# Kernel optimization log

Measured on AMD Instinct MI355X. Metric: run time of the kernel, lower is better.

Reference implementation:

```python
import jax, jax.numpy as jnp
import numpy as np

V = 50000
K = 24
NB = 10
P = (K - 1) * 9  # 207 pose-blend coefficients
# canonical SMPL kinematic tree (parent[0] is unused / root)
SMPL_PARENT = np.array([0, 0, 0, 0, 1, 2, 3, 4, 5, 6, 7, 8, 9, 9, 9, 12, 13, 14, 16, 17, 18, 19, 20, 21], dtype=np.int64)


def setup_inputs() -> dict:
    key = jax.random.key(0)
    ks = jax.random.split(key, 8)
    betas = jax.random.normal(ks[0], (NB,), dtype=jnp.float32)
    pose = jax.random.normal(ks[1], (K, 3), dtype=jnp.float32) * 0.3
    trans = jax.random.normal(ks[2], (3,), dtype=jnp.float32)
    shapedirs = jax.random.normal(ks[3], (V, 3, NB), dtype=jnp.float32) * 0.01
    v_template = jax.random.normal(ks[4], (V, 3), dtype=jnp.float32)
    J_regressor = jax.random.uniform(ks[5], (K, V), dtype=jnp.float32)
    J_regressor = J_regressor / jnp.sum(J_regressor, axis=1, keepdims=True)
    weights = jax.random.uniform(ks[6], (V, K), dtype=jnp.float32)
    weights = weights / jnp.sum(weights, axis=1, keepdims=True)
    posedirs = jax.random.normal(ks[7], (V, 3, P), dtype=jnp.float32) * 0.01
    return {"betas": betas, "pose": pose, "trans": trans, "shapedirs": shapedirs,
            "v_template": v_template, "J_regressor": J_regressor, "weights": weights,
            "posedirs": posedirs, "parent": SMPL_PARENT}


def rodrigues(r):
    """Axis-angle [K,3] -> rotation matrices [K,3,3]."""
    theta = jnp.linalg.norm(r + 1e-8, axis=-1, keepdims=True)  # [K,1]
    r_hat = r / theta
    x, y, z = r_hat[:, 0], r_hat[:, 1], r_hat[:, 2]
    zero = jnp.zeros_like(x)
    m = jnp.stack([zero, -z, y, z, zero, -x, -y, x, zero], axis=1).reshape(-1, 3, 3)
    cos = jnp.cos(theta)[:, :, None]
    sin = jnp.sin(theta)[:, :, None]
    eye = jnp.eye(3, dtype=r.dtype)[None]
    outer = r_hat[:, :, None] * r_hat[:, None, :]
    return cos * eye + (1.0 - cos) * outer + sin * m


def smpl_forward(betas, pose, trans, shapedirs, v_template, J_regressor, weights, posedirs, parent):
    parent = np.asarray(parent)
    nJ = parent.shape[0]
    v_shaped = jnp.einsum('vki,i->vk', shapedirs, betas) + v_template  # [V,3]
    J = J_regressor @ v_shaped                                          # [K,3]
    R = rodrigues(pose.reshape(-1, 3))                                  # [K,3,3]
    lrotmin = (R[1:] - jnp.eye(3, dtype=R.dtype)[None]).reshape(-1)     # [207]
    v_posed = v_shaped + jnp.einsum('vkp,p->vk', posedirs, lrotmin)

    bottom = jnp.array([[0.0, 0.0, 0.0, 1.0]], dtype=R.dtype)
    def make_A(Ri, t):  # [3,3],[3] -> [4,4]
        return jnp.concatenate([jnp.concatenate([Ri, t[:, None]], axis=1), bottom], axis=0)

    G = [make_A(R[0], J[0])]
    for i in range(1, nJ):  # fixed 24-joint tree, small static loop
        p = int(parent[i])
        G.append(G[p] @ make_A(R[i], J[i] - J[p]))
    stacked = jnp.stack(G, axis=0)                                      # [K,4,4]

    Jh = jnp.concatenate([J, jnp.zeros((nJ, 1), dtype=J.dtype)], axis=1)[:, :, None]  # [K,4,1]
    corr = stacked @ Jh                                                 # [K,4,1]
    pack = jnp.concatenate([jnp.zeros((nJ, 4, 3), dtype=J.dtype), corr], axis=2)
    results = stacked - pack                                            # [K,4,4]

    T = jnp.einsum('vj,jab->vab', weights, results)                     # [V,4,4]
    rest = jnp.concatenate([v_posed, jnp.ones((v_posed.shape[0], 1), dtype=v_posed.dtype)], axis=1)
    v = jnp.einsum('vab,vb->va', T, rest)[:, :3]
    return v + trans[None, :]


def reference(betas, pose, trans, shapedirs, v_template, J_regressor, weights, posedirs, parent):
    return smpl_forward(betas, pose, trans, shapedirs, v_template, J_regressor, weights, posedirs, parent)
```

## Files before the change

### kernel.cpp

```cpp
#include <hip/hip_runtime.h>

#define NV 50000
#define NJ 24
#define NBETA 10
#define NP 207
#define NROWS 150000
#define ROWGROUPS 37500

#define K1_BLOCKS 196

#define PARTIAL_OFF 0
#define LROT_OFF    14336
#define M_OFF       14592

__device__ const int d_par[NJ] = {0,0,0,0,1,2,3,4,5,6,7,8,9,9,9,12,13,14,16,17,18,19,20,21};
__device__ const int d_lvl[NJ] = {0,1,1,1,2,2,2,3,3,3,4,4,4,4,4,5,5,5,6,6,7,7,8,8};

__global__ __launch_bounds__(256) void k1_partialJ(
    const float* __restrict__ betas, const float* __restrict__ shapedirs,
    const float* __restrict__ v_template, const float* __restrict__ Jreg,
    float* __restrict__ ws)
{
    __shared__ float sd[256 * 30];
    __shared__ float vt[256 * 3];
    __shared__ float bet[NBETA];
    __shared__ float red[4 * 72];

    const int t = threadIdx.x;
    const int blk = blockIdx.x;
    if (t < NBETA) bet[t] = betas[t];

    const int vbase = blk * 256;
    const int nv    = min(256, NV - vbase);
    {
        const int nf4 = (nv * 30) >> 2;
        const float4* sdg = (const float4*)(shapedirs + (size_t)vbase * 30);
        for (int i = t; i < nf4; i += 256) ((float4*)sd)[i] = sdg[i];
        const float* vtg = v_template + (size_t)vbase * 3;
        const int nf3 = nv * 3;
        for (int i = t; i < nf3; i += 256) vt[i] = vtg[i];
    }
    __syncthreads();

    float accJ[72];
#pragma unroll
    for (int q = 0; q < 72; q++) accJ[q] = 0.f;

    const int v = vbase + t;
    if (v < NV) {
        float vs0 = vt[t * 3 + 0], vs1 = vt[t * 3 + 1], vs2 = vt[t * 3 + 2];
#pragma unroll
        for (int i = 0; i < NBETA; i++) {
            const float b = bet[i];
            vs0 += sd[t * 30 + 0 * 10 + i] * b;
            vs1 += sd[t * 30 + 1 * 10 + i] * b;
            vs2 += sd[t * 30 + 2 * 10 + i] * b;
        }
#pragma unroll
        for (int j = 0; j < NJ; j++) {
            const float w = Jreg[(size_t)j * NV + v];
            accJ[j * 3 + 0] += w * vs0;
            accJ[j * 3 + 1] += w * vs1;
            accJ[j * 3 + 2] += w * vs2;
        }
    }

    const int lane = t & 63, wv = t >> 6;
#pragma unroll
    for (int q = 0; q < 72; q++) {
        float x = accJ[q];
#pragma unroll
        for (int m = 1; m < 64; m <<= 1) x += __shfl_xor(x, m);
        if (lane == 0) red[wv * 72 + q] = x;
    }
    __syncthreads();
    if (t < 72)
        ws[PARTIAL_OFF + blk * 72 + t] = red[t] + red[72 + t] + red[144 + t] + red[216 + t];
}

__global__ __launch_bounds__(256) void k2_small(
    const float* __restrict__ pose, float* __restrict__ ws)
{
    __shared__ float Jl[NJ * 3];
    __shared__ float Rl[NJ * 9];
    __shared__ float Gl[NJ * 12];
    const int t = threadIdx.x;

    if (t < 72) {
        float s0 = 0.f, s1 = 0.f;
        for (int b = 0; b < K1_BLOCKS; b += 2) {
            s0 += ws[PARTIAL_OFF + b * 72 + t];
            s1 += ws[PARTIAL_OFF + (b + 1) * 72 + t];
        }
        Jl[t] = s0 + s1;
    }
    __syncthreads();

    if (t < NJ) {
        const float x = pose[t * 3 + 0], y = pose[t * 3 + 1], z = pose[t * 3 + 2];
        const float ex = x + 1e-8f, ey = y + 1e-8f, ez = z + 1e-8f;
        const float theta = sqrtf(ex * ex + ey * ey + ez * ez);
        const float inv = 1.f / theta;
        const float rx = x * inv, ry = y * inv, rz = z * inv;
        const float c = cosf(theta), s = sinf(theta), omc = 1.f - c;
        float R[9];
        R[0] = c + omc * rx * rx;      R[1] = omc * rx * ry - s * rz; R[2] = omc * rx * rz + s * ry;
        R[3] = omc * ry * rx + s * rz; R[4] = c + omc * ry * ry;      R[5] = omc * ry * rz - s * rx;
        R[6] = omc * rz * rx - s * ry; R[7] = omc * rz * ry + s * rx; R[8] = c + omc * rz * rz;
#pragma unroll
        for (int q = 0; q < 9; q++) Rl[t * 9 + q] = R[q];
        if (t >= 1) {
#pragma unroll
            for (int q = 0; q < 9; q++)
                ws[LROT_OFF + (t - 1) * 9 + q] = R[q] - ((q == 0 || q == 4 || q == 8) ? 1.f : 0.f);
        }
    }
    __syncthreads();

    for (int L = 0; L < 9; L++) {
        if (t < NJ && d_lvl[t] == L) {
            if (t == 0) {
#pragma unroll
                for (int r = 0; r < 3; r++) {
                    Gl[r * 4 + 0] = Rl[r * 3 + 0];
                    Gl[r * 4 + 1] = Rl[r * 3 + 1];
                    Gl[r * 4 + 2] = Rl[r * 3 + 2];
                    Gl[r * 4 + 3] = Jl[r];
                }
            } else {
                const int p = d_par[t];
                const float tx = Jl[t * 3 + 0] - Jl[p * 3 + 0];
                const float ty = Jl[t * 3 + 1] - Jl[p * 3 + 1];
                const float tz = Jl[t * 3 + 2] - Jl[p * 3 + 2];
#pragma unroll
                for (int r = 0; r < 3; r++) {
                    const float g0 = Gl[p * 12 + r * 4 + 0];
                    const float g1 = Gl[p * 12 + r * 4 + 1];
                    const float g2 = Gl[p * 12 + r * 4 + 2];
                    const float g3 = Gl[p * 12 + r * 4 + 3];
                    Gl[t * 12 + r * 4 + 0] = g0 * Rl[t * 9 + 0] + g1 * Rl[t * 9 + 3] + g2 * Rl[t * 9 + 6];
                    Gl[t * 12 + r * 4 + 1] = g0 * Rl[t * 9 + 1] + g1 * Rl[t * 9 + 4] + g2 * Rl[t * 9 + 7];
                    Gl[t * 12 + r * 4 + 2] = g0 * Rl[t * 9 + 2] + g1 * Rl[t * 9 + 5] + g2 * Rl[t * 9 + 8];
                    Gl[t * 12 + r * 4 + 3] = g0 * tx + g1 * ty + g2 * tz + g3;
                }
            }
        }
        __syncthreads();
    }

    if (t < NJ) {
        const float jx = Jl[t * 3 + 0], jy = Jl[t * 3 + 1], jz = Jl[t * 3 + 2];
#pragma unroll
        for (int r = 0; r < 3; r++) {
            const float g0 = Gl[t * 12 + r * 4 + 0];
            const float g1 = Gl[t * 12 + r * 4 + 1];
            const float g2 = Gl[t * 12 + r * 4 + 2];
            const float g3 = Gl[t * 12 + r * 4 + 3];
            ws[M_OFF + t * 12 + r * 4 + 0] = g0;
            ws[M_OFF + t * 12 + r * 4 + 1] = g1;
            ws[M_OFF + t * 12 + r * 4 + 2] = g2;
            ws[M_OFF + t * 12 + r * 4 + 3] = g3 - (g0 * jx + g1 * jy + g2 * jz);
        }
    }
}

__global__ __launch_bounds__(256) void k3a_posegemv(
    const float* __restrict__ betas, const float* __restrict__ shapedirs,
    const float* __restrict__ v_template, const float* __restrict__ posedirs,
    const float* __restrict__ ws, float* __restrict__ out)
{
    const int t = threadIdx.x;
    const int lane = t & 63, wv = t >> 6;
    const int l16 = lane & 15, g = lane >> 4;

    float lrk[12];
#pragma unroll
    for (int k = 0; k < 12; k++) lrk[k] = ws[LROT_OFF + k * 16 + l16];
    const float lr12 = (l16 < 15) ? ws[LROT_OFF + 192 + l16] : 0.f;
    const float bet  = (l16 < NBETA) ? betas[l16] : 0.f;

    const int wgid    = blockIdx.x * 4 + wv;
    const int wstride = gridDim.x * 4;

    for (int grp = wgid; grp < ROWGROUPS; grp += wstride) {
        const int row = grp * 4 + g;
        const float* pd = posedirs + (size_t)row * NP;
        float acc = 0.f;
#pragma unroll
        for (int k = 0; k < 12; k++) acc += pd[k * 16 + l16] * lrk[k];
        if (l16 < 15)    acc += pd[192 + l16] * lr12;
        if (l16 < NBETA) acc += shapedirs[(size_t)row * NBETA + l16] * bet;
#pragma unroll
        for (int m = 1; m < 16; m <<= 1) acc += __shfl_xor(acc, m);
        if (l16 == 0) out[row] = acc + v_template[row];
    }
}

__global__ __launch_bounds__(256) void k3b_skin(
    const float* __restrict__ trans, const float* __restrict__ weights,
    const float* __restrict__ ws, float* __restrict__ out)
{
    __shared__ float Ml[288];
    const int t = threadIdx.x;
    Ml[t] = ws[M_OFF + t];
    if (t < 32) Ml[256 + t] = ws[M_OFF + 256 + t];
    __syncthreads();

    const int v = blockIdx.x * 256 + t;
    if (v >= NV) return;

    const float4* w4 = (const float4*)(weights + (size_t)v * 24);
    float wj[24];
#pragma unroll
    for (int q = 0; q < 6; q++) {
        const float4 w = w4[q];
        wj[q * 4 + 0] = w.x; wj[q * 4 + 1] = w.y;
        wj[q * 4 + 2] = w.z; wj[q * 4 + 3] = w.w;
    }

    float T[12];
#pragma unroll
    for (int q = 0; q < 12; q++) T[q] = 0.f;
#pragma unroll
    for (int j = 0; j < NJ; j++) {
        const float w = wj[j];
#pragma unroll
        for (int q = 0; q < 12; q++) T[q] += w * Ml[j * 12 + q];
    }

    const float p0 = out[(size_t)v * 3 + 0];
    const float p1 = out[(size_t)v * 3 + 1];
    const float p2 = out[(size_t)v * 3 + 2];
    out[(size_t)v * 3 + 0] = T[0] * p0 + T[1] * p1 + T[2]  * p2 + T[3]  + trans[0];
    out[(size_t)v * 3 + 1] = T[4] * p0 + T[5] * p1 + T[6]  * p2 + T[7]  + trans[1];
    out[(size_t)v * 3 + 2] = T[8] * p0 + T[9] * p1 + T[10] * p2 + T[11] + trans[2];
}

extern "C" void kernel_launch(void* const* d_in, const int* in_sizes, int n_in,
                              void* d_out, int out_size, void* d_ws, size_t ws_size,
                              hipStream_t stream) {
    const float* betas      = (const float*)d_in[0];
    const float* pose       = (const float*)d_in[1];
    const float* trans      = (const float*)d_in[2];
    const float* shapedirs  = (const float*)d_in[3];
    const float* v_template = (const float*)d_in[4];
    const float* Jreg       = (const float*)d_in[5];
    const float* weights    = (const float*)d_in[6];
    const float* posedirs   = (const float*)d_in[7];
    float* ws  = (float*)d_ws;
    float* out = (float*)d_out;

    k1_partialJ<<<dim3(K1_BLOCKS), dim3(256), 0, stream>>>(betas, shapedirs, v_template, Jreg, ws);
    k2_small<<<dim3(1), dim3(256), 0, stream>>>(pose, ws);
    k3a_posegemv<<<dim3(2048), dim3(256), 0, stream>>>(betas, shapedirs, v_template, posedirs, ws, out);
    k3b_skin<<<dim3((NV + 255) / 256), dim3(256), 0, stream>>>(trans, weights, ws, out);
}
```

Before: 57.03 us.

## Fuse pose-blend GEMV and skinning into one kernel via shared memory

Merges the posedirs GEMV kernel and the skinning kernel into one launch. Each block computes 32 vertices' posed positions into shared memory, then skins them, so the intermediate no longer round-trips through global memory and one launch is removed. Each wave now handles two rows per iteration with loads issued up front to raise memory-level parallelism. In exchange, only 32 threads per block do the skinning stage while the rest sit idle after the barrier.

```diff
diff --git a/kernel.cpp b/kernel.cpp
--- a/kernel.cpp
+++ b/kernel.cpp
@@ -5,9 +5,13 @@
 #define NBETA 10
 #define NP 207
 #define NROWS 150000
-#define ROWGROUPS 37500
 
 #define K1_BLOCKS 196
+
+#define VPB 32
+#define RPB 96
+#define GPB 24
+#define K3_BLOCKS 1563
 
 #define PARTIAL_OFF 0
 #define LROT_OFF    14336
@@ -164,14 +168,22 @@
     }
 }
 
-__global__ __launch_bounds__(256) void k3a_posegemv(
-    const float* __restrict__ betas, const float* __restrict__ shapedirs,
-    const float* __restrict__ v_template, const float* __restrict__ posedirs,
+__global__ __launch_bounds__(256) void k3_fused(
+    const float* __restrict__ betas, const float* __restrict__ trans,
+    const float* __restrict__ shapedirs, const float* __restrict__ v_template,
+    const float* __restrict__ weights, const float* __restrict__ posedirs,
     const float* __restrict__ ws, float* __restrict__ out)
 {
+    __shared__ float vposed[RPB];
+    __shared__ float Ml[288];
+
     const int t = threadIdx.x;
     const int lane = t & 63, wv = t >> 6;
     const int l16 = lane & 15, g = lane >> 4;
+    const int blk = blockIdx.x;
+
+    Ml[t] = ws[M_OFF + t];
+    if (t < 32) Ml[256 + t] = ws[M_OFF + 256 + t];
 
     float lrk[12];
 #pragma unroll
@@ -179,61 +191,83 @@
     const float lr12 = (l16 < 15) ? ws[LROT_OFF + 192 + l16] : 0.f;
     const float bet  = (l16 < NBETA) ? betas[l16] : 0.f;
 
-    const int wgid    = blockIdx.x * 4 + wv;
-    const int wstride = gridDim.x * 4;
-
-    for (int grp = wgid; grp < ROWGROUPS; grp += wstride) {
-        const int row = grp * 4 + g;
-        const float* pd = posedirs + (size_t)row * NP;
-        float acc = 0.f;
-#pragma unroll
-        for (int k = 0; k < 12; k++) acc += pd[k * 16 + l16] * lrk[k];
-        if (l16 < 15)    acc += pd[192 + l16] * lr12;
-        if (l16 < NBETA) acc += shapedirs[(size_t)row * NBETA + l16] * bet;
-#pragma unroll
-        for (int m = 1; m < 16; m <<= 1) acc += __shfl_xor(acc, m);
-        if (l16 == 0) out[row] = acc + v_template[row];
-    }
-}
-
-__global__ __launch_bounds__(256) void k3b_skin(
-    const float* __restrict__ trans, const float* __restrict__ weights,
-    const float* __restrict__ ws, float* __restrict__ out)
-{
-    __shared__ float Ml[288];
-    const int t = threadIdx.x;
-    Ml[t] = ws[M_OFF + t];
-    if (t < 32) Ml[256 + t] = ws[M_OFF + 256 + t];
-    __syncthreads();
-
-    const int v = blockIdx.x * 256 + t;
-    if (v >= NV) return;
-
-    const float4* w4 = (const float4*)(weights + (size_t)v * 24);
-    float wj[24];
-#pragma unroll
-    for (int q = 0; q < 6; q++) {
-        const float4 w = w4[q];
-        wj[q * 4 + 0] = w.x; wj[q * 4 + 1] = w.y;
-        wj[q * 4 + 2] = w.z; wj[q * 4 + 3] = w.w;
-    }
-
-    float T[12];
-#pragma unroll
-    for (int q = 0; q < 12; q++) T[q] = 0.f;
-#pragma unroll
-    for (int j = 0; j < NJ; j++) {
-        const float w = wj[j];
-#pragma unroll
-        for (int q = 0; q < 12; q++) T[q] += w * Ml[j * 12 + q];
-    }
-
-    const float p0 = out[(size_t)v * 3 + 0];
-    const float p1 = out[(size_t)v * 3 + 1];
-    const float p2 = out[(size_t)v * 3 + 2];
-    out[(size_t)v * 3 + 0] = T[0] * p0 + T[1] * p1 + T[2]  * p2 + T[3]  + trans[0];
-    out[(size_t)v * 3 + 1] = T[4] * p0 + T[5] * p1 + T[6]  * p2 + T[7]  + trans[1];
-    out[(size_t)v * 3 + 2] = T[8] * p0 + T[9] * p1 + T[10] * p2 + T[11] + trans[2];
+    const int gbase = blk * GPB + wv * 6;
+#pragma unroll
+    for (int i = 0; i < 6; i += 2) {
+        const int rowA = (gbase + i) * 4 + g;
+        const int rowB = rowA + 4;
+        const bool okA = rowA < NROWS;
+        const bool okB = rowB < NROWS;
+
+        float va[12], vb[12];
+        float tA = 0.f, tB = 0.f, sA = 0.f, sB = 0.f;
+        if (okA) {
+            const float* pa = posedirs + (size_t)rowA * NP;
+#pragma unroll
+            for (int k = 0; k < 12; k++) va[k] = pa[k * 16 + l16];
+            if (l16 < 15)    tA = pa[192 + l16];
+            if (l16 < NBETA) sA = shapedirs[(size_t)rowA * NBETA + l16];
+        } else {
+#pragma unroll
+            for (int k = 0; k < 12; k++) va[k] = 0.f;
+        }
+        if (okB) {
+            const float* pb = posedirs + (size_t)rowB * NP;
+#pragma unroll
+            for (int k = 0; k < 12; k++) vb[k] = pb[k * 16 + l16];
+            if (l16 < 15)    tB = pb[192 + l16];
+            if (l16 < NBETA) sB = shapedirs[(size_t)rowB * NBETA + l16];
+        } else {
+#pragma unroll
+            for (int k = 0; k < 12; k++) vb[k] = 0.f;
+        }
+
+        float accA = tA * lr12 + sA * bet;
+        float accB = tB * lr12 + sB * bet;
+#pragma unroll
+        for (int k = 0; k < 12; k++) accA += va[k] * lrk[k];
+#pragma unroll
+        for (int k = 0; k < 12; k++) accB += vb[k] * lrk[k];
+#pragma unroll
+        for (int m = 1; m < 16; m <<= 1) {
+            accA += __shfl_xor(accA, m);
+            accB += __shfl_xor(accB, m);
+        }
+        if (l16 == 0) {
+            if (okA) vposed[rowA - blk * RPB] = accA + v_template[rowA];
+            if (okB) vposed[rowB - blk * RPB] = accB + v_template[rowB];
+        }
+    }
+    __syncthreads();
+
+    if (t < VPB) {
+        const int v = blk * VPB + t;
+        if (v < NV) {
+            const float4* w4 = (const float4*)(weights + (size_t)v * 24);
+            float wj[24];
+#pragma unroll
+            for (int q = 0; q < 6; q++) {
+                const float4 w = w4[q];
+                wj[q * 4 + 0] = w.x; wj[q * 4 + 1] = w.y;
+                wj[q * 4 + 2] = w.z; wj[q * 4 + 3] = w.w;
+            }
+            float T[12];
+#pragma unroll
+            for (int q = 0; q < 12; q++) T[q] = 0.f;
+#pragma unroll
+            for (int j = 0; j < NJ; j++) {
+                const float w = wj[j];
+#pragma unroll
+                for (int q = 0; q < 12; q++) T[q] += w * Ml[j * 12 + q];
+            }
+            const float p0 = vposed[t * 3 + 0];
+            const float p1 = vposed[t * 3 + 1];
+            const float p2 = vposed[t * 3 + 2];
+            out[(size_t)v * 3 + 0] = T[0] * p0 + T[1] * p1 + T[2]  * p2 + T[3]  + trans[0];
+            out[(size_t)v * 3 + 1] = T[4] * p0 + T[5] * p1 + T[6]  * p2 + T[7]  + trans[1];
+            out[(size_t)v * 3 + 2] = T[8] * p0 + T[9] * p1 + T[10] * p2 + T[11] + trans[2];
+        }
+    }
 }
 
 extern "C" void kernel_launch(void* const* d_in, const int* in_sizes, int n_in,
@@ -252,6 +286,6 @@
 
     k1_partialJ<<<dim3(K1_BLOCKS), dim3(256), 0, stream>>>(betas, shapedirs, v_template, Jreg, ws);
     k2_small<<<dim3(1), dim3(256), 0, stream>>>(pose, ws);
-    k3a_posegemv<<<dim3(2048), dim3(256), 0, stream>>>(betas, shapedirs, v_template, posedirs, ws, out);
-    k3b_skin<<<dim3((NV + 255) / 256), dim3(256), 0, stream>>>(trans, weights, ws, out);
-}
+    k3_fused<<<dim3(K3_BLOCKS), dim3(256), 0, stream>>>(
+        betas, trans, shapedirs, v_template, weights, posedirs, ws, out);
+}
```

New measurement: 55.69 us. -2.4%, faster.

## Stage posedirs tiles in LDS with coalesced float4 loads for pose GEMV

Applied to the files above, without the earlier changes.

The pose-blend GEMV now uses one block per 64 rows. Each block copies its contiguous 64x207 posedirs slab into shared memory with fully coalesced float4 loads, then computes row dot products from LDS, with 4 threads per row each covering 52 coefficients. The aim is to replace the previous strided 16-lane per-row loads, which wasted bandwidth on a non-multiple-of-16 row length. The k2 joint reduction is also split across 216 threads, and lrot is padded to 208 entries so it can be read as float4. The tradeoff is heavy LDS use per block (about 53KB), which limits occupancy, plus LDS bank conflicts from the 207-float row stride.

```diff
diff --git a/kernel.cpp b/kernel.cpp
--- a/kernel.cpp
+++ b/kernel.cpp
@@ -5,13 +5,14 @@
 #define NBETA 10
 #define NP 207
 #define NROWS 150000
-#define ROWGROUPS 37500
 
 #define K1_BLOCKS 196
 
+#define K3A_BLOCKS 2344
+
 #define PARTIAL_OFF 0
-#define LROT_OFF    14336
-#define M_OFF       14592
+#define LROT_OFF    14592
+#define M_OFF       14848
 
 __device__ const int d_par[NJ] = {0,0,0,0,1,2,3,4,5,6,7,8,9,9,9,12,13,14,16,17,18,19,20,21};
 __device__ const int d_lvl[NJ] = {0,1,1,1,2,2,2,3,3,3,4,4,4,4,4,5,5,5,6,6,7,7,8,8};
@@ -84,16 +85,20 @@
     __shared__ float Jl[NJ * 3];
     __shared__ float Rl[NJ * 9];
     __shared__ float Gl[NJ * 12];
-    const int t = threadIdx.x;
-
-    if (t < 72) {
-        float s0 = 0.f, s1 = 0.f;
-        for (int b = 0; b < K1_BLOCKS; b += 2) {
-            s0 += ws[PARTIAL_OFF + b * 72 + t];
-            s1 += ws[PARTIAL_OFF + (b + 1) * 72 + t];
-        }
-        Jl[t] = s0 + s1;
-    }
+    __shared__ float lrotl[NP];
+    __shared__ float cs[3 * 72];
+    const int t = threadIdx.x;
+
+    if (t < 216) {
+        const int q = t % 72, chunk = t / 72;
+        const int b0 = chunk * 66;
+        const int b1 = min(K1_BLOCKS, b0 + 66);
+        float s = 0.f;
+        for (int b = b0; b < b1; b++) s += ws[PARTIAL_OFF + b * 72 + q];
+        cs[chunk * 72 + q] = s;
+    }
+    __syncthreads();
+    if (t < 72) Jl[t] = cs[t] + cs[72 + t] + cs[144 + t];
     __syncthreads();
 
     if (t < NJ) {
@@ -112,10 +117,12 @@
         if (t >= 1) {
 #pragma unroll
             for (int q = 0; q < 9; q++)
-                ws[LROT_OFF + (t - 1) * 9 + q] = R[q] - ((q == 0 || q == 4 || q == 8) ? 1.f : 0.f);
-        }
-    }
-    __syncthreads();
+                lrotl[(t - 1) * 9 + q] = R[q] - ((q == 0 || q == 4 || q == 8) ? 1.f : 0.f);
+        }
+    }
+    __syncthreads();
+
+    if (t < 208) ws[LROT_OFF + t] = (t < NP) ? lrotl[t] : 0.f;
 
     for (int L = 0; L < 9; L++) {
         if (t < NJ && d_lvl[t] == L) {
@@ -164,35 +171,58 @@
     }
 }
 
-__global__ __launch_bounds__(256) void k3a_posegemv(
+__global__ __launch_bounds__(256, 2) void k3a_posegemv(
     const float* __restrict__ betas, const float* __restrict__ shapedirs,
     const float* __restrict__ v_template, const float* __restrict__ posedirs,
     const float* __restrict__ ws, float* __restrict__ out)
 {
-    const int t = threadIdx.x;
-    const int lane = t & 63, wv = t >> 6;
-    const int l16 = lane & 15, g = lane >> 4;
-
-    float lrk[12];
-#pragma unroll
-    for (int k = 0; k < 12; k++) lrk[k] = ws[LROT_OFF + k * 16 + l16];
-    const float lr12 = (l16 < 15) ? ws[LROT_OFF + 192 + l16] : 0.f;
-    const float bet  = (l16 < NBETA) ? betas[l16] : 0.f;
-
-    const int wgid    = blockIdx.x * 4 + wv;
-    const int wstride = gridDim.x * 4;
-
-    for (int grp = wgid; grp < ROWGROUPS; grp += wstride) {
-        const int row = grp * 4 + g;
-        const float* pd = posedirs + (size_t)row * NP;
-        float acc = 0.f;
-#pragma unroll
-        for (int k = 0; k < 12; k++) acc += pd[k * 16 + l16] * lrk[k];
-        if (l16 < 15)    acc += pd[192 + l16] * lr12;
-        if (l16 < NBETA) acc += shapedirs[(size_t)row * NBETA + l16] * bet;
-#pragma unroll
-        for (int m = 1; m < 16; m <<= 1) acc += __shfl_xor(acc, m);
-        if (l16 == 0) out[row] = acc + v_template[row];
+    __shared__ float4 tile4[3313];
+    __shared__ float sdt[640];
+    __shared__ float lrotl[208];
+    __shared__ float part[256];
+    __shared__ float betl[NBETA];
+
+    const int t = threadIdx.x;
+    const int blk = blockIdx.x;
+    const int rbase = blk * 64;
+    const int rows = min(64, NROWS - rbase);
+    const int nf4 = (rows * 207) >> 2;
+
+    const float4* gp = (const float4*)posedirs + (size_t)blk * 3312;
+    const float4 z4 = {0.f, 0.f, 0.f, 0.f};
+    float4 r[13];
+#pragma unroll
+    for (int i = 0; i < 13; i++) {
+        const int idx = i * 256 + t;
+        r[i] = (idx < nf4) ? gp[idx] : z4;
+    }
+#pragma unroll
+    for (int i = 0; i < 13; i++) {
+        const int idx = i * 256 + t;
+        if (idx < nf4) tile4[idx] = r[i];
+    }
+    if (t < ((rows * 10) >> 2))
+        ((float4*)sdt)[t] = ((const float4*)(shapedirs + (size_t)rbase * 10))[t];
+    if (t < 52) ((float4*)lrotl)[t] = ((const float4*)(ws + LROT_OFF))[t];
+    if (t < NBETA) betl[t] = betas[t];
+    if (t == 0) tile4[3312] = z4;
+    __syncthreads();
+
+    const int row = t & 63, q = t >> 6;
+    const float* tile = (const float*)tile4;
+    const float* rp = tile + row * 207 + q * 52;
+    const float* lp = lrotl + q * 52;
+    float p = 0.f;
+#pragma unroll
+    for (int j = 0; j < 52; j++) p += rp[j] * lp[j];
+    part[q * 64 + row] = p;
+    __syncthreads();
+
+    if (t < 64 && rbase + t < NROWS) {
+        float vp = part[t] + part[64 + t] + part[128 + t] + part[192 + t];
+#pragma unroll
+        for (int c = 0; c < NBETA; c++) vp += sdt[t * 10 + c] * betl[c];
+        out[rbase + t] = vp + v_template[rbase + t];
     }
 }
 
@@ -252,6 +282,7 @@
 
     k1_partialJ<<<dim3(K1_BLOCKS), dim3(256), 0, stream>>>(betas, shapedirs, v_template, Jreg, ws);
     k2_small<<<dim3(1), dim3(256), 0, stream>>>(pose, ws);
-    k3a_posegemv<<<dim3(2048), dim3(256), 0, stream>>>(betas, shapedirs, v_template, posedirs, ws, out);
+    k3a_posegemv<<<dim3(K3A_BLOCKS), dim3(256), 0, stream>>>(
+        betas, shapedirs, v_template, posedirs, ws, out);
     k3b_skin<<<dim3((NV + 255) / 256), dim3(256), 0, stream>>>(trans, weights, ws, out);
 }
```

New measurement: 82.81 us. +45.2%, slower.
